# Kernel tuning notes

Hardware: AMD Instinct MI355X
Metric: run time of the kernel (lower is better)

The kernel has to match this reference:

```python
import jax, jax.numpy as jnp
import numpy as np

B, H, W = 2, 192, 192
DIM, HEADS, WS = 192, 6, 16
NT, RD, GS = 128, 20, 128
MLP_HID, TD_F, KS = 384, 48, 5
EPS = 1e-5


def _layernorm(x, g, b):
    m = jnp.mean(x, -1, keepdims=True)
    v = jnp.var(x, -1, keepdims=True)
    return (x - m) / jnp.sqrt(v + EPS) * g + b


def _l2n(x):
    return x / jnp.maximum(jnp.linalg.norm(x, axis=-1, keepdims=True), 1e-12)


def _rpi(ws):
    coords = np.stack(np.meshgrid(np.arange(ws), np.arange(ws), indexing='ij'))
    cf = coords.reshape(2, -1)
    rc = (cf[:, :, None] - cf[:, None, :]).transpose(1, 2, 0)
    rc[..., 0] += ws - 1
    rc[..., 1] += ws - 1
    rc[..., 0] *= 2 * ws - 1
    return rc.sum(-1)  # (ws*ws, ws*ws)


RPI = _rpi(WS)


def _win_attn(qkv, rpb, proj_w, h, w):
    # plain W-MSA (shift_size = 0 -> no mask, no roll)
    b, n, c3 = qkv.shape
    c = c3 // 3
    hd = c // HEADS
    nw = WS * WS
    xw = qkv.reshape(b, h // WS, WS, w // WS, WS, c3).transpose(0, 1, 3, 2, 4, 5).reshape(-1, nw, c3)
    bw = xw.shape[0]
    q, k, v = xw.reshape(bw, nw, 3, HEADS, hd).transpose(2, 0, 3, 1, 4)
    attn = (q * hd ** -0.5) @ k.swapaxes(-2, -1)  # (bw, heads, nw, nw)
    bias = rpb[RPI.reshape(-1)].reshape(nw, nw, HEADS).transpose(2, 0, 1)
    attn = jax.nn.softmax(attn + bias[None])
    out = (attn @ v).swapaxes(1, 2).reshape(bw, nw, c) @ proj_w
    out = out.reshape(b, h // WS, w // WS, WS, WS, c).transpose(0, 1, 3, 2, 4, 5).reshape(b, n, c)
    return out


def _atd_ca(x, td, wq, wk, wv, scale_p):
    q = _l2n(x @ wq)   # (b,n,rd)
    k = _l2n(td @ wk)  # (b,m,rd)
    v = td @ wv        # (b,m,c)
    scale = 1.0 + jnp.clip(scale_p, 0.0, 3.0) * np.log(NT)
    attn = jax.nn.softmax((q @ k.swapaxes(-2, -1)) * scale)  # (b,n,m)
    return attn @ v, attn


def _ac_msa(qkv, tk_id, proj_w):
    b, n, c3 = qkv.shape
    c = c3 // 3
    gs = min(n, GS)
    ng = (n + gs - 1) // gs
    pad = ng * gs - n
    idx = jnp.argsort(tk_id, axis=-1)          # sort tokens by category id
    inv = jnp.argsort(idx, axis=-1)            # inverse permutation
    sq = jnp.take_along_axis(qkv, idx[..., None], axis=1)
    if pad > 0:
        sq = jnp.concatenate([sq, sq[:, n - pad:n][:, ::-1]], axis=1)
    q, k, v = sq.reshape(b, ng, gs, 3, HEADS, c // HEADS).transpose(3, 0, 1, 4, 2, 5)
    attn = jax.nn.softmax((q @ k.swapaxes(-2, -1)) * (c // HEADS) ** -0.5)
    out = (attn @ v).transpose(0, 1, 3, 2, 4).reshape(b, ng * gs, c)[:, :n]
    out = jnp.take_along_axis(out, inv[..., None], axis=1)
    return out @ proj_w


def _convffn(x, x_td, w1, dw, w2, h, w):
    y = jnp.concatenate([jax.nn.gelu(x @ w1, approximate=False), x_td], axis=-1)
    b, n, ch = y.shape
    img = y.swapaxes(1, 2).reshape(b, ch, h, w)
    p = (KS - 1) // 2
    conv = jax.lax.conv_general_dilated(img, dw, (1, 1), [(p, p), (p, p)],
                                        dimension_numbers=('NCHW', 'OIHW', 'NCHW'),
                                        feature_group_count=ch)
    conv = jax.nn.gelu(conv, approximate=False).reshape(b, ch, n).swapaxes(1, 2)
    return (y + conv) @ w2


def setup_inputs():
    key = jax.random.key(0)
    ks = jax.random.split(key, 16)
    p = lambda k, s: jax.random.normal(k, s, jnp.float32) * 0.02
    return {
        'x': jax.random.normal(ks[0], (B, H * W, DIM), jnp.float32),
        'td': jax.random.normal(ks[1], (B, NT, DIM), jnp.float32),
        'norm1_g': jnp.ones((DIM,), jnp.float32), 'norm1_b': jnp.zeros((DIM,), jnp.float32),
        'norm2_g': jnp.ones((DIM,), jnp.float32), 'norm2_b': jnp.zeros((DIM,), jnp.float32),
        'wqkv': p(ks[2], (DIM, 3 * DIM)),
        'rpb': p(ks[3], ((2 * WS - 1) ** 2, HEADS)),
        'win_proj': p(ks[4], (DIM, DIM)),
        'atd_wq': p(ks[5], (DIM, RD)),
        'atd_wk': p(ks[6], (DIM, RD)),
        'atd_wv': p(ks[7], (DIM, DIM)),
        'atd_scale': jnp.ones((1,), jnp.float32),
        'aca_proj': p(ks[8], (DIM, DIM)),
        'fc_td_w': p(ks[9], (DIM, TD_F)),
        'ffn_w1': p(ks[10], (DIM, MLP_HID)),
        'ffn_dw': p(ks[11], (MLP_HID + TD_F, 1, KS, KS)),
        'ffn_w2': p(ks[12], (MLP_HID + TD_F, DIM)),
        'h': H, 'w': W,
    }


def reference(x, td, norm1_g, norm1_b, norm2_g, norm2_b, wqkv, rpb, win_proj,
              atd_wq, atd_wk, atd_wv, atd_scale, aca_proj, fc_td_w,
              ffn_w1, ffn_dw, ffn_w2, h, w):
    shortcut = x
    xn = _layernorm(x, norm1_g, norm1_b)
    qkv = xn @ wqkv  # (b, n, 3c)
    x_atd, sim = _atd_ca(xn, td, atd_wq, atd_wk, atd_wv, atd_scale)
    x_aca = _ac_msa(qkv, jnp.argmax(sim, axis=-1), aca_proj)
    x_win = _win_attn(qkv, rpb, win_proj, h, w)
    x = shortcut + x_win + x_atd + x_aca
    x_td = sim @ (td @ fc_td_w)  # (b, n, td_f): dictionary features routed by cross-attn weights
    x = x + _convffn(_layernorm(x, norm2_g, norm2_b), x_td, ffn_w1, ffn_dw, ffn_w2, h, w)
    return x
```

## Files before the change

kernel.cpp:

```cpp
#include <hip/hip_runtime.h>
#include <hip/hip_bf16.h>
#include <math.h>

#define NTOK 36864
#define NTOT 73728
#define CDIM 192
#define C3   576
#define NH   6
#define HD   32
#define RD   20
#define NTD  128
#define GSZ  128
#define NGRP 288
#define MLP  384
#define TDF  48
#define CH   432
#define RAWLD 384

typedef __hip_bfloat16 bf16;
typedef __attribute__((ext_vector_type(8))) short short8;
typedef __attribute__((ext_vector_type(4))) float f32x4;

__device__ __forceinline__ float gelu_f(float x) {
    float u = x * (1.5957691216f + 0.0713548162f * x * x);
    return x / (1.0f + __expf(-u));
}

__device__ __forceinline__ unsigned short f32_to_bf16u(float f) {
    unsigned int u = __float_as_uint(f);
    u = (u + 0x7FFFu + ((u >> 16) & 1u)) >> 16;
    return (unsigned short)u;
}

__device__ __forceinline__ unsigned pack2bf(float a, float b) {
    return (unsigned)f32_to_bf16u(a) | ((unsigned)f32_to_bf16u(b) << 16);
}

__device__ __forceinline__ float bfbits2f(unsigned short u) {
    return __uint_as_float(((unsigned)u) << 16);
}

__global__ void pack_bt(const float* __restrict__ src, bf16* __restrict__ dst,
                        int K, int N, int ldk, int koff) {
    int i = blockIdx.x * 256 + threadIdx.x;
    if (i >= K * N) return;
    int k = i / N, n = i - k * N;
    dst[(long)n * ldk + koff + k] = __float2bfloat16(src[i]);
}

template<int WF32>
__global__ void ln_kernel(const float* __restrict__ x, const float* __restrict__ g,
                          const float* __restrict__ be, float* __restrict__ outf,
                          bf16* __restrict__ outh) {
    long tok = (long)blockIdx.x * 4 + (threadIdx.x >> 6);
    int lane = threadIdx.x & 63;
    const float* row = x + tok * CDIM;
    float v0 = row[lane], v1 = row[lane + 64], v2 = row[lane + 128];
    float s  = v0 + v1 + v2;
    float ss = v0 * v0 + v1 * v1 + v2 * v2;
    #pragma unroll
    for (int o = 32; o > 0; o >>= 1) {
        s  += __shfl_down(s, o);
        ss += __shfl_down(ss, o);
    }
    s = __shfl(s, 0); ss = __shfl(ss, 0);
    float mean = s * (1.0f / 192.0f);
    float var  = ss * (1.0f / 192.0f) - mean * mean;
    float rstd = rsqrtf(var + 1e-5f);
    float r0 = (v0 - mean) * rstd * g[lane]       + be[lane];
    float r1 = (v1 - mean) * rstd * g[lane + 64]  + be[lane + 64];
    float r2 = (v2 - mean) * rstd * g[lane + 128] + be[lane + 128];
    if (WF32) {
        float* orow = outf + tok * CDIM;
        orow[lane] = r0; orow[lane + 64] = r1; orow[lane + 128] = r2;
    }
    bf16* hrow = outh + tok * CDIM;
    hrow[lane]       = __float2bfloat16(r0);
    hrow[lane + 64]  = __float2bfloat16(r1);
    hrow[lane + 128] = __float2bfloat16(r2);
}

#define LDT 72
template<int ACC, int GELU, int BF16OUT, int CHUNK8, int ADDX, int PL8OUT = 0>
__global__ void __launch_bounds__(256) gemm_bt(
        const bf16* __restrict__ A, const bf16* __restrict__ Bt,
        void* __restrict__ Cv, const float* __restrict__ Xadd,
        int M, int N, int K, int lda, int ldbt, int ldc) {
    __shared__ short As[128 * LDT];
    __shared__ short Bs[64 * LDT];
    int tid  = threadIdx.x;
    int lane = tid & 63;
    int w    = tid >> 6;
    int wr = w >> 1, wc = w & 1;
    int row0 = blockIdx.y * 128, col0 = blockIdx.x * 64;
    int fr = lane & 15, fq = lane >> 4;
    f32x4 acc[4][2];
    #pragma unroll
    for (int m = 0; m < 4; ++m)
        #pragma unroll
        for (int n = 0; n < 2; ++n) acc[m][n] = (f32x4)(0.0f);

    int sa_row = tid >> 3;
    int sa_kc  = (tid & 7) * 8;
    int sb_col = tid & 63;
    int sb_kb  = (tid >> 6) * 16;
    bool cok = (col0 + sb_col) < N;

    for (int k0 = 0; k0 < K; k0 += 64) {
        __syncthreads();
        int kk = k0 + sa_kc;
        #pragma unroll
        for (int p = 0; p < 4; ++p) {
            int r = sa_row + p * 32;
            short8 v = (short8)(0);
            if (kk + 8 <= K) {
                const bf16* src;
                if (CHUNK8)
                    src = A + ((long)(kk >> 3) * NTOT + row0 + r) * 8;
                else
                    src = A + (long)(row0 + r) * lda + kk;
                v = *(const short8*)src;
            } else if (!CHUNK8 && kk < K) {
                #pragma unroll
                for (int i = 0; i < 8; ++i)
                    v[i] = (kk + i < K) ? *(const short*)&A[(long)(row0 + r) * lda + kk + i]
                                        : (short)0;
            }
            *(short8*)&As[r * LDT + sa_kc] = v;
        }
        {
            short8 v0 = (short8)(0), v1 = (short8)(0);
            if (cok) {
                const bf16* src = Bt + (long)(col0 + sb_col) * ldbt + k0 + sb_kb;
                v0 = *(const short8*)src;
                v1 = *(const short8*)(src + 8);
            }
            *(short8*)&Bs[sb_col * LDT + sb_kb]     = v0;
            *(short8*)&Bs[sb_col * LDT + sb_kb + 8] = v1;
        }
        __syncthreads();
        short8 af[4][2], bf_[2][2];
        #pragma unroll
        for (int m = 0; m < 4; ++m) {
            int r = wr * 64 + m * 16 + fr;
            af[m][0] = *(const short8*)&As[r * LDT + fq * 8];
            af[m][1] = *(const short8*)&As[r * LDT + 32 + fq * 8];
        }
        #pragma unroll
        for (int n = 0; n < 2; ++n) {
            int c = wc * 32 + n * 16 + fr;
            bf_[n][0] = *(const short8*)&Bs[c * LDT + fq * 8];
            bf_[n][1] = *(const short8*)&Bs[c * LDT + 32 + fq * 8];
        }
        #pragma unroll
        for (int m = 0; m < 4; ++m)
            #pragma unroll
            for (int n = 0; n < 2; ++n) {
                acc[m][n] = __builtin_amdgcn_mfma_f32_16x16x32_bf16(
                                af[m][0], bf_[n][0], acc[m][n], 0, 0, 0);
                acc[m][n] = __builtin_amdgcn_mfma_f32_16x16x32_bf16(
                                af[m][1], bf_[n][1], acc[m][n], 0, 0, 0);
            }
    }
    #pragma unroll
    for (int m = 0; m < 4; ++m) {
        #pragma unroll
        for (int n = 0; n < 2; ++n) {
            int gc = col0 + wc * 32 + n * 16 + fr;
            if (gc >= N) continue;
            #pragma unroll
            for (int r = 0; r < 4; ++r) {
                int gr = row0 + wr * 64 + m * 16 + fq * 4 + r;
                float vv = acc[m][n][r];
                if (GELU) vv = gelu_f(vv);
                if (BF16OUT) {
                    long o;
                    if (PL8OUT) o = ((long)(gc >> 3) * NTOT + gr) * 8 + (gc & 7);
                    else        o = (long)gr * ldc + gc;
                    ((bf16*)Cv)[o] = __float2bfloat16(vv);
                } else {
                    long o = (long)gr * ldc + gc;
                    float* Cc = (float*)Cv;
                    if (ADDX) Cc[o] = Xadd[o] + vv;
                    else if (ACC) Cc[o] += vv;
                    else Cc[o] = vv;
                }
            }
        }
    }
}

template<int ACC, int GELU>
__global__ void __launch_bounds__(256) gemm_kernel(
        const float* __restrict__ A, const float* __restrict__ B,
        float* __restrict__ Cc, int M, int N, int K, int lda, int ldb, int ldc) {
    __shared__ float As[16][68];
    __shared__ float Bs[16][68];
    int tid = threadIdx.x;
    int tr = tid >> 4, tc = tid & 15;
    int row0 = blockIdx.y * 64, col0 = blockIdx.x * 64;
    float acc[4][4] = {};
    int lm = tid >> 4;
    int lk = tid & 15;
    int bk = tid >> 6;
    int bn = tid & 63;
    for (int k0 = 0; k0 < K; k0 += 16) {
        #pragma unroll
        for (int i = 0; i < 4; ++i) {
            int m = lm + i * 16;
            int gr = row0 + m;
            As[lk][m] = (gr < M) ? A[(long)gr * lda + (k0 + lk)] : 0.0f;
        }
        #pragma unroll
        for (int i = 0; i < 4; ++i) {
            int kk = bk + i * 4;
            int gc = col0 + bn;
            Bs[kk][bn] = (gc < N) ? B[(long)(k0 + kk) * ldb + gc] : 0.0f;
        }
        __syncthreads();
        #pragma unroll
        for (int kk = 0; kk < 16; ++kk) {
            float4 av = *(const float4*)&As[kk][tr * 4];
            float4 bv = *(const float4*)&Bs[kk][tc * 4];
            float a[4] = {av.x, av.y, av.z, av.w};
            float b[4] = {bv.x, bv.y, bv.z, bv.w};
            #pragma unroll
            for (int i = 0; i < 4; ++i)
                #pragma unroll
                for (int j = 0; j < 4; ++j)
                    acc[i][j] = fmaf(a[i], b[j], acc[i][j]);
        }
        __syncthreads();
    }
    #pragma unroll
    for (int i = 0; i < 4; ++i) {
        int gr = row0 + tr * 4 + i;
        if (gr >= M) continue;
        #pragma unroll
        for (int j = 0; j < 4; ++j) {
            int gc = col0 + tc * 4 + j;
            if (gc >= N) continue;
            float v = acc[i][j];
            if (GELU) v = gelu_f(v);
            long o = (long)gr * ldc + gc;
            if (ACC) Cc[o] += v; else Cc[o] = v;
        }
    }
}

__global__ void __launch_bounds__(256) qn_kernel(
        const float* __restrict__ xn, const float* __restrict__ awq,
        float* __restrict__ qn) {
    __shared__ float aw[192 * RD];
    __shared__ float xs[256 * 33];
    int tid = threadIdx.x;
    long tok0 = (long)blockIdx.x * 256;
    for (int e = tid; e < 192 * RD; e += 256) aw[e] = awq[e];
    float acc[RD];
    #pragma unroll
    for (int j = 0; j < RD; ++j) acc[j] = 0.0f;
    for (int kc = 0; kc < 192; kc += 32) {
        __syncthreads();
        for (int e = tid; e < 256 * 32; e += 256) {
            int tk = e >> 5, kk = e & 31;
            xs[tk * 33 + kk] = xn[(tok0 + tk) * CDIM + kc + kk];
        }
        __syncthreads();
        #pragma unroll 8
        for (int kk = 0; kk < 32; ++kk) {
            float v = xs[tid * 33 + kk];
            const float* ar = &aw[(kc + kk) * RD];
            #pragma unroll
            for (int j = 0; j < RD; ++j) acc[j] = fmaf(v, ar[j], acc[j]);
        }
    }
    float ss = 0.0f;
    #pragma unroll
    for (int j = 0; j < RD; ++j) ss += acc[j] * acc[j];
    float inv = 1.0f / fmaxf(sqrtf(ss), 1e-12f);
    float* orow = qn + (tok0 + tid) * RD;
    #pragma unroll
    for (int j = 0; j < RD; ++j) orow[j] = acc[j] * inv;
}

__global__ void l2n_kernel(float* __restrict__ d, int nrows) {
    int i = blockIdx.x * blockDim.x + threadIdx.x;
    if (i >= nrows) return;
    float* r = d + (long)i * RD;
    float ss = 0.0f;
    #pragma unroll
    for (int k = 0; k < RD; ++k) ss += r[k] * r[k];
    float inv = 1.0f / fmaxf(sqrtf(ss), 1e-12f);
    #pragma unroll
    for (int k = 0; k < RD; ++k) r[k] *= inv;
}

__global__ void __launch_bounds__(128) sim_kernel(
        const float* __restrict__ qn, const float* __restrict__ kn,
        const float* __restrict__ scale_p, bf16* __restrict__ sim,
        int* __restrict__ tkid) {
    int tok = blockIdx.x;
    int b = tok / NTOK;
    int j = threadIdx.x;
    __shared__ float qv[RD];
    __shared__ float wred[4];
    __shared__ int   wredi[2];
    if (j < RD) qv[j] = qn[(long)tok * RD + j];
    __syncthreads();
    const float* kr = kn + ((long)b * NTD + j) * RD;
    float s = 0.0f;
    #pragma unroll
    for (int r = 0; r < RD; ++r) s = fmaf(qv[r], kr[r], s);
    float scl = 1.0f + fminf(fmaxf(scale_p[0], 0.0f), 3.0f) * logf(128.0f);
    s *= scl;
    float m = s; int mi = j;
    #pragma unroll
    for (int o = 32; o > 0; o >>= 1) {
        float om = __shfl_down(m, o); int oi = __shfl_down(mi, o);
        if (om > m || (om == m && oi < mi)) { m = om; mi = oi; }
    }
    int wv = j >> 6;
    if ((j & 63) == 0) { wred[wv] = m; wredi[wv] = mi; }
    __syncthreads();
    float m0 = wred[0], m1 = wred[1];
    float gm; int gi;
    if (m1 > m0) { gm = m1; gi = wredi[1]; } else { gm = m0; gi = wredi[0]; }
    float p = __expf(s - gm);
    float t = p;
    #pragma unroll
    for (int o = 32; o > 0; o >>= 1) t += __shfl_down(t, o);
    if ((j & 63) == 0) wred[2 + wv] = t;
    __syncthreads();
    float tot = wred[2] + wred[3];
    sim[(long)tok * NTD + j] = __float2bfloat16(p / tot);
    if (j == 0) tkid[tok] = gi;
}

__global__ void hist_kernel(const int* __restrict__ tkid, int* __restrict__ hist) {
    int tile = blockIdx.x;
    int tid = threadIdx.x;
    __shared__ int h[NTD];
    h[tid] = 0;
    __syncthreads();
    atomicAdd(&h[tkid[tile * GSZ + tid]], 1);
    __syncthreads();
    hist[tile * NTD + tid] = h[tid];
}

__global__ void scan_kernel(int* __restrict__ hist) {
    int b = blockIdx.x;
    int c = threadIdx.x;
    __shared__ int tot[NTD];
    __shared__ int base[NTD];
    int run = 0;
    for (int t = 0; t < NGRP; ++t) {
        int id = (b * NGRP + t) * NTD + c;
        int v = hist[id];
        hist[id] = run;
        run += v;
    }
    tot[c] = run;
    __syncthreads();
    if (c == 0) {
        int a = 0;
        for (int i = 0; i < NTD; ++i) { base[i] = a; a += tot[i]; }
    }
    __syncthreads();
    int bc = base[c];
    for (int t = 0; t < NGRP; ++t)
        hist[(b * NGRP + t) * NTD + c] += bc;
}

__global__ void scatter_kernel(const int* __restrict__ tkid, const int* __restrict__ hist,
                               int* __restrict__ idxs) {
    int tile = blockIdx.x;
    int b = tile / NGRP;
    int gl = tile % NGRP;
    int tid = threadIdx.x;
    __shared__ int cats[GSZ];
    int cat = tkid[tile * GSZ + tid];
    cats[tid] = cat;
    __syncthreads();
    int rank = 0;
    for (int j = 0; j < tid; ++j) rank += (cats[j] == cat) ? 1 : 0;
    int pos = hist[tile * NTD + cat] + rank;
    idxs[b * NTOK + pos] = gl * GSZ + tid;
}

#define VLDW 264
#define VLDA 136


__global__ void __launch_bounds__(256) win_mfma(
        const bf16* __restrict__ qkv, const float* __restrict__ rpb,
        bf16* __restrict__ raw) {
    int t2  = blockIdx.x;
    int h   = t2 % NH;
    int wid = t2 / NH;
    int b = wid / 144;
    int wrem = wid % 144;
    int wy = wrem / 12, wx = wrem % 12;
    long base_tok = (long)b * NTOK;

    __shared__ short Kt[256 * 40];
    __shared__ short Vt[32 * VLDW];
    __shared__ float rb[961];

    int tid = threadIdx.x;
    int lane = tid & 63;
    int wv = tid >> 6;
    int fr = lane & 15, fq = lane >> 4;
    const float scl = 0.17677669529663687f;

    for (int i = tid; i < 961; i += 256) rb[i] = rpb[i * NH + h];

    short8 qf[4];
    #pragma unroll
    for (int m = 0; m < 4; ++m) {
        int q = wv * 64 + m * 16 + fr;
        long nq = base_tok + (long)(wy * 16 + (q >> 4)) * 192 + (wx * 16 + (q & 15));
        qf[m] = *(const short8*)(qkv + nq * C3 + h * HD + fq * 8);
    }

    {
        int s_ = tid >> 2, ch = tid & 3;
        #pragma unroll
        for (int t = 0; t < 4; ++t) {
            int p = t * 64 + s_;
            long nk = base_tok + (long)(wy * 16 + (p >> 4)) * 192 + (wx * 16 + (p & 15));
            const bf16* kb = qkv + nk * C3 + CDIM + h * HD + ch * 8;
            *(short8*)&Kt[p * 40 + ch * 8] = *(const short8*)kb;
            short8 vv = *(const short8*)(kb + CDIM);
            #pragma unroll
            for (int i = 0; i < 8; ++i)
                Vt[(ch * 8 + i) * VLDW + p] = vv[i];
        }
    }
    __syncthreads();

    f32x4 acc[4][2];
    float lst[4];
    #pragma unroll
    for (int m = 0; m < 4; ++m) {
        acc[m][0] = (f32x4)(0.0f); acc[m][1] = (f32x4)(0.0f);
        lst[m] = 0.0f;
    }

    for (int t = 0; t < 4; ++t) {
        short8 ak[4], av[2][2];
        #pragma unroll
        for (int c = 0; c < 4; ++c)
            ak[c] = *(const short8*)&Kt[(t * 64 + c * 16 + fr) * 40 + fq * 8];
        #pragma unroll
        for (int n = 0; n < 2; ++n)
            #pragma unroll
            for (int ks = 0; ks < 2; ++ks)
                av[n][ks] = *(const short8*)&Vt[(n * 16 + fr) * VLDW + t * 64 + ks * 32 + fq * 8];

        #pragma unroll
        for (int m = 0; m < 4; ++m) {
            int q = wv * 64 + m * 16 + fr;
            int iy = q >> 4, ix = q & 15;
            int bxb = ix + 15 - 4 * fq;
            float s[4][4];
            #pragma unroll
            for (int c = 0; c < 4; ++c) {
                f32x4 s4 = (f32x4)(0.0f);
                s4 = __builtin_amdgcn_mfma_f32_16x16x32_bf16(ak[c], qf[m], s4, 0, 0, 0);
                const float* rbp = &rb[(iy + 15 - (t * 4 + c)) * 31 + bxb];
                #pragma unroll
                for (int r = 0; r < 4; ++r)
                    s[c][r] = s4[r] * scl + rbp[-r];
            }
            float ps = 0.0f;
            #pragma unroll
            for (int c = 0; c < 4; ++c)
                #pragma unroll
                for (int r = 0; r < 4; ++r) {
                    float p = __expf(s[c][r]);
                    s[c][r] = p;
                    ps += p;
                }
            ps += __shfl_xor(ps, 16);
            ps += __shfl_xor(ps, 32);
            lst[m] += ps;
            unsigned pk[4][2];
            #pragma unroll
            for (int c = 0; c < 4; ++c) {
                pk[c][0] = pack2bf(s[c][0], s[c][1]);
                pk[c][1] = pack2bf(s[c][2], s[c][3]);
            }
            #pragma unroll
            for (int ks = 0; ks < 2; ++ks) {
                unsigned u[4];
                #pragma unroll
                for (int jj = 0; jj < 4; ++jj) {
                    int src = fr + 16 * (2 * (fq & 1) + (jj >> 1));
                    unsigned lo = (unsigned)__shfl((int)pk[2 * ks][jj & 1], src);
                    unsigned hi = (unsigned)__shfl((int)pk[2 * ks + 1][jj & 1], src);
                    u[jj] = (fq & 2) ? hi : lo;
                }
                short8 pb;
                #pragma unroll
                for (int jj = 0; jj < 4; ++jj) {
                    pb[2 * jj]     = (short)(u[jj] & 0xFFFF);
                    pb[2 * jj + 1] = (short)(u[jj] >> 16);
                }
                #pragma unroll
                for (int n = 0; n < 2; ++n)
                    acc[m][n] = __builtin_amdgcn_mfma_f32_16x16x32_bf16(
                                    av[n][ks], pb, acc[m][n], 0, 0, 0);
            }
        }
    }
    #pragma unroll
    for (int m = 0; m < 4; ++m) {
        int q = wv * 64 + m * 16 + fr;
        long nq = base_tok + (long)(wy * 16 + (q >> 4)) * 192 + (wx * 16 + (q & 15));
        float inv = 1.0f / lst[m];
        #pragma unroll
        for (int n = 0; n < 2; ++n) {
            uint2 wv2;
            wv2.x = pack2bf(acc[m][n][0] * inv, acc[m][n][1] * inv);
            wv2.y = pack2bf(acc[m][n][2] * inv, acc[m][n][3] * inv);
            *(uint2*)(raw + nq * RAWLD + h * HD + n * 16 + 4 * fq) = wv2;
        }
    }
}

__global__ void __launch_bounds__(128) aca_mfma(
        const bf16* __restrict__ qkv, const int* __restrict__ idxs,
        bf16* __restrict__ raw) {
    int t2   = blockIdx.x;
    int h    = t2 % NH;
    int grp  = t2 / NH;
    int b = grp / NGRP;
    int g = grp % NGRP;
    long btok = (long)b * NTOK;

    __shared__ short Kt[128 * 40];
    __shared__ short Vt[32 * VLDA];
    __shared__ int   sidx[GSZ];

    int tid = threadIdx.x;
    int lane = tid & 63;
    int half = tid >> 6;
    int fr = lane & 15, fq = lane >> 4;
    const float scl = 0.17677669529663687f;

    sidx[tid] = idxs[btok + g * GSZ + tid];
    __syncthreads();

    short8 qf[4];
    #pragma unroll
    for (int m = 0; m < 4; ++m) {
        long n = btok + sidx[half * 64 + m * 16 + fr];
        qf[m] = *(const short8*)(qkv + n * C3 + h * HD + fq * 8);
    }

    {
        int s_ = tid >> 1, hf = tid & 1;
        int d0 = hf * 16;
        #pragma unroll
        for (int t = 0; t < 2; ++t) {
            int p = t * 64 + s_;
            long n = btok + sidx[p];
            const bf16* kb = qkv + n * C3 + CDIM + h * HD + d0;
            *(short8*)&Kt[p * 40 + d0]     = *(const short8*)kb;
            *(short8*)&Kt[p * 40 + d0 + 8] = *(const short8*)(kb + 8);
            short8 v0 = *(const short8*)(kb + CDIM);
            short8 v1 = *(const short8*)(kb + CDIM + 8);
            #pragma unroll
            for (int i = 0; i < 8; ++i) {
                Vt[(d0 + i) * VLDA + p]     = v0[i];
                Vt[(d0 + 8 + i) * VLDA + p] = v1[i];
            }
        }
    }
    __syncthreads();

    f32x4 acc[4][2];
    float lst[4];
    #pragma unroll
    for (int m = 0; m < 4; ++m) {
        acc[m][0] = (f32x4)(0.0f); acc[m][1] = (f32x4)(0.0f);
        lst[m] = 0.0f;
    }

    for (int t = 0; t < 2; ++t) {
        short8 ak[4], av[2][2];
        #pragma unroll
        for (int c = 0; c < 4; ++c)
            ak[c] = *(const short8*)&Kt[(t * 64 + c * 16 + fr) * 40 + fq * 8];
        #pragma unroll
        for (int n = 0; n < 2; ++n)
            #pragma unroll
            for (int ks = 0; ks < 2; ++ks)
                av[n][ks] = *(const short8*)&Vt[(n * 16 + fr) * VLDA + t * 64 + ks * 32 + fq * 8];

        #pragma unroll
        for (int m = 0; m < 4; ++m) {
            float s[4][4];
            #pragma unroll
            for (int c = 0; c < 4; ++c) {
                f32x4 s4 = (f32x4)(0.0f);
                s4 = __builtin_amdgcn_mfma_f32_16x16x32_bf16(ak[c], qf[m], s4, 0, 0, 0);
                #pragma unroll
                for (int r = 0; r < 4; ++r) s[c][r] = s4[r] * scl;
            }
            float ps = 0.0f;
            #pragma unroll
            for (int c = 0; c < 4; ++c)
                #pragma unroll
                for (int r = 0; r < 4; ++r) {
                    float p = __expf(s[c][r]);
                    s[c][r] = p;
                    ps += p;
                }
            ps += __shfl_xor(ps, 16);
            ps += __shfl_xor(ps, 32);
            lst[m] += ps;
            unsigned pk[4][2];
            #pragma unroll
            for (int c = 0; c < 4; ++c) {
                pk[c][0] = pack2bf(s[c][0], s[c][1]);
                pk[c][1] = pack2bf(s[c][2], s[c][3]);
            }
            #pragma unroll
            for (int ks = 0; ks < 2; ++ks) {
                unsigned u[4];
                #pragma unroll
                for (int jj = 0; jj < 4; ++jj) {
                    int src = fr + 16 * (2 * (fq & 1) + (jj >> 1));
                    unsigned lo = (unsigned)__shfl((int)pk[2 * ks][jj & 1], src);
                    unsigned hi = (unsigned)__shfl((int)pk[2 * ks + 1][jj & 1], src);
                    u[jj] = (fq & 2) ? hi : lo;
                }
                short8 pb;
                #pragma unroll
                for (int jj = 0; jj < 4; ++jj) {
                    pb[2 * jj]     = (short)(u[jj] & 0xFFFF);
                    pb[2 * jj + 1] = (short)(u[jj] >> 16);
                }
                #pragma unroll
                for (int n = 0; n < 2; ++n)
                    acc[m][n] = __builtin_amdgcn_mfma_f32_16x16x32_bf16(
                                    av[n][ks], pb, acc[m][n], 0, 0, 0);
            }
        }
    }
    #pragma unroll
    for (int m = 0; m < 4; ++m) {
        long n = btok + sidx[half * 64 + m * 16 + fr];
        float inv = 1.0f / lst[m];
        #pragma unroll
        for (int nn = 0; nn < 2; ++nn) {
            uint2 wv2;
            wv2.x = pack2bf(acc[m][nn][0] * inv, acc[m][nn][1] * inv);
            wv2.y = pack2bf(acc[m][nn][2] * inv, acc[m][nn][3] * inv);
            *(uint2*)(raw + n * RAWLD + CDIM + h * HD + nn * 16 + 4 * fq) = wv2;
        }
    }
}

__global__ void xtdcopy_kernel(const bf16* __restrict__ xtd, bf16* __restrict__ y) {
    long tok = (long)blockIdx.x * 256 + threadIdx.x;
    const uint4* src = (const uint4*)(xtd + tok * TDF);
    #pragma unroll
    for (int j = 0; j < 6; ++j)
        *(uint4*)(y + ((long)(48 + j) * NTOT + tok) * 8) = src[j];
}

#define CPS 1296
__global__ void __launch_bounds__(256) conv_kernel(
        const bf16* __restrict__ y, const float* __restrict__ dw,
        bf16* __restrict__ zc) {
    int bid = blockIdx.x;
    int ck   = bid % 54;
    int tile = (bid / 54) % 36;
    int b    = bid / (54 * 36);
    int ty = tile / 6, tx = tile % 6;
    int c0 = ck * 8;
    __shared__ float ys[8 * CPS];
    __shared__ float wt[8 * 25];
    int tid = threadIdx.x;
    const bf16* ypl = y + ((long)ck * NTOT + (long)b * NTOK) * 8;
    for (int p = tid; p < 1296; p += 256) {
        int ly = p / 36, lx = p - ly * 36;
        int gy = ty * 32 + ly - 2, gx = tx * 32 + lx - 2;
        float f[8];
        if (gy >= 0 && gy < 192 && gx >= 0 && gx < 192) {
            short8 hv = *(const short8*)(ypl + (long)(gy * 192 + gx) * 8);
            #pragma unroll
            for (int i = 0; i < 8; ++i) f[i] = bfbits2f((unsigned short)hv[i]);
        } else {
            #pragma unroll
            for (int i = 0; i < 8; ++i) f[i] = 0.0f;
        }
        #pragma unroll
        for (int i = 0; i < 8; ++i) ys[i * CPS + p] = f[i];
    }
    for (int e = tid; e < 200; e += 256) wt[e] = dw[c0 * 25 + e];
    __syncthreads();
    int col = tid & 31, r4 = tid >> 5;
    int py0 = r4 * 4;
    long tok0 = (long)b * NTOK + (long)(ty * 32 + py0) * 192 + tx * 32 + col;
    unsigned hh[4][4];
    for (int c = 0; c < 8; ++c) {
        const float* yc = &ys[c * CPS];
        float w[25];
        #pragma unroll
        for (int t = 0; t < 25; ++t) w[t] = wt[c * 25 + t];
        float a[4] = {0.0f, 0.0f, 0.0f, 0.0f};
        #pragma unroll
        for (int dy2 = 0; dy2 < 8; ++dy2) {
            float rv[5];
            #pragma unroll
            for (int dx = 0; dx < 5; ++dx)
                rv[dx] = yc[(py0 + dy2) * 36 + col + dx];
            #pragma unroll
            for (int i = 0; i < 4; ++i) {
                int dy = dy2 - i;
                if (dy >= 0 && dy < 5) {
                    #pragma unroll
                    for (int dx = 0; dx < 5; ++dx)
                        a[i] = fmaf(rv[dx], w[dy * 5 + dx], a[i]);
                }
            }
        }
        #pragma unroll
        for (int i = 0; i < 4; ++i) {
            float center = yc[(py0 + i + 2) * 36 + col + 2];
            unsigned short hsh = f32_to_bf16u(center + gelu_f(a[i]));
            if (c & 1) hh[i][c >> 1] |= ((unsigned)hsh) << 16;
            else       hh[i][c >> 1] = (unsigned)hsh;
        }
    }
    #pragma unroll
    for (int i = 0; i < 4; ++i) {
        long tok = tok0 + (long)i * 192;
        *(uint4*)(zc + ((long)ck * NTOT + tok) * 8) =
            make_uint4(hh[i][0], hh[i][1], hh[i][2], hh[i][3]);
    }
}

extern "C" void kernel_launch(void* const* d_in, const int* in_sizes, int n_in,
                              void* d_out, int out_size, void* d_ws, size_t ws_size,
                              hipStream_t stream) {
    (void)in_sizes; (void)n_in; (void)out_size; (void)ws_size;
    const float* x     = (const float*)d_in[0];
    const float* td    = (const float*)d_in[1];
    const float* n1g   = (const float*)d_in[2];
    const float* n1b   = (const float*)d_in[3];
    const float* n2g   = (const float*)d_in[4];
    const float* n2b   = (const float*)d_in[5];
    const float* wqkv  = (const float*)d_in[6];
    const float* rpb   = (const float*)d_in[7];
    const float* wproj = (const float*)d_in[8];
    const float* awq   = (const float*)d_in[9];
    const float* awk   = (const float*)d_in[10];
    const float* awv   = (const float*)d_in[11];
    const float* ascl  = (const float*)d_in[12];
    const float* aproj = (const float*)d_in[13];
    const float* fcw   = (const float*)d_in[14];
    const float* w1    = (const float*)d_in[15];
    const float* dw    = (const float*)d_in[16];
    const float* w2    = (const float*)d_in[17];
    float* out = (float*)d_out;

    char* ws = (char*)d_ws;
    size_t off = 0;
    auto alloc = [&](size_t bytes) -> char* {
        char* p = ws + off;
        off += (bytes + 255) & ~(size_t)255;
        return p;
    };
    bf16*  qkv  = (bf16*)alloc((size_t)NTOT * C3 * 2);
    float* xn   = (float*)alloc((size_t)NTOT * CDIM * 4);
    bf16*  xnh  = (bf16*)alloc((size_t)NTOT * CDIM * 2);
    float* qn   = (float*)alloc((size_t)NTOT * RD * 4);
    bf16*  simb = (bf16*)alloc((size_t)NTOT * NTD * 2);
    bf16*  xtd  = (bf16*)alloc((size_t)NTOT * TDF * 2);
    float* kn   = (float*)alloc((size_t)2 * NTD * RD * 4);
    float* vtd  = (float*)alloc((size_t)2 * NTD * CDIM * 4);
    float* tdf  = (float*)alloc((size_t)2 * NTD * TDF * 4);
    bf16*  vtdT = (bf16*)alloc((size_t)2 * CDIM * NTD * 2);
    bf16*  tdfT = (bf16*)alloc((size_t)2 * TDF * NTD * 2);
    bf16*  wqkvT= (bf16*)alloc((size_t)C3 * CDIM * 2);
    bf16*  projT= (bf16*)alloc((size_t)CDIM * 384 * 2);
    bf16*  w1T  = (bf16*)alloc((size_t)MLP * CDIM * 2);
    bf16*  w2T  = (bf16*)alloc((size_t)CDIM * 448 * 2);
    int*   tkid = (int*)alloc((size_t)NTOT * 4);
    int*   idxs = (int*)alloc((size_t)NTOT * 4);
    int*   hist = (int*)alloc((size_t)576 * NTD * 4);
    bf16*  y    = qkv;
    bf16*  raw  = (bf16*)xn;
    bf16*  zc   = (bf16*)xn;

    pack_bt<<<(192 * 576 + 255) / 256, 256, 0, stream>>>(wqkv, wqkvT, 192, 576, 192, 0);
    pack_bt<<<(192 * 192 + 255) / 256, 256, 0, stream>>>(wproj, projT, 192, 192, 384, 0);
    pack_bt<<<(192 * 192 + 255) / 256, 256, 0, stream>>>(aproj, projT, 192, 192, 384, 192);
    pack_bt<<<(192 * 384 + 255) / 256, 256, 0, stream>>>(w1, w1T, 192, 384, 192, 0);
    hipMemsetAsync(w2T, 0, (size_t)CDIM * 448 * 2, stream);
    pack_bt<<<(432 * 192 + 255) / 256, 256, 0, stream>>>(w2, w2T, 432, 192, 448, 0);

    ln_kernel<1><<<NTOT / 4, 256, 0, stream>>>(x, n1g, n1b, xn, xnh);

    gemm_bt<0,0,1,0,0><<<dim3(9, 576), 256, 0, stream>>>(
        xnh, wqkvT, qkv, nullptr, NTOT, C3, CDIM, CDIM, CDIM, C3);

    qn_kernel<<<NTOT / 256, 256, 0, stream>>>(xn, awq, qn);

    gemm_kernel<0,0><<<dim3(1, 4), 256, 0, stream>>>(td, awk, kn, 2 * NTD, RD, CDIM, CDIM, RD, RD);
    gemm_kernel<0,0><<<dim3(3, 4), 256, 0, stream>>>(td, awv, vtd, 2 * NTD, CDIM, CDIM, CDIM, CDIM, CDIM);
    gemm_kernel<0,0><<<dim3(1, 4), 256, 0, stream>>>(td, fcw, tdf, 2 * NTD, TDF, CDIM, CDIM, TDF, TDF);
    l2n_kernel<<<1, 256, 0, stream>>>(kn, 2 * NTD);
    for (int b = 0; b < 2; ++b) {
        pack_bt<<<(NTD * CDIM + 255) / 256, 256, 0, stream>>>(
            vtd + (size_t)b * NTD * CDIM, vtdT + (size_t)b * CDIM * NTD, NTD, CDIM, NTD, 0);
        pack_bt<<<(NTD * TDF + 255) / 256, 256, 0, stream>>>(
            tdf + (size_t)b * NTD * TDF, tdfT + (size_t)b * TDF * NTD, NTD, TDF, NTD, 0);
    }

    sim_kernel<<<NTOT, 128, 0, stream>>>(qn, kn, ascl, simb, tkid);

    for (int b = 0; b < 2; ++b) {
        gemm_bt<0,0,0,0,1><<<dim3(3, 288), 256, 0, stream>>>(
            simb + (size_t)b * NTOK * NTD, vtdT + (size_t)b * CDIM * NTD,
            out + (size_t)b * NTOK * CDIM, x + (size_t)b * NTOK * CDIM,
            NTOK, CDIM, NTD, NTD, NTD, CDIM);
        gemm_bt<0,0,1,0,0><<<dim3(1, 288), 256, 0, stream>>>(
            simb + (size_t)b * NTOK * NTD, tdfT + (size_t)b * TDF * NTD,
            xtd + (size_t)b * NTOK * TDF, nullptr, NTOK, TDF, NTD, NTD, NTD, TDF);
    }

    hist_kernel<<<576, 128, 0, stream>>>(tkid, hist);
    scan_kernel<<<2, 128, 0, stream>>>(hist);
    scatter_kernel<<<576, 128, 0, stream>>>(tkid, hist, idxs);

    win_mfma<<<288 * NH, 256, 0, stream>>>(qkv, rpb, raw);
    aca_mfma<<<576 * NH, 128, 0, stream>>>(qkv, idxs, raw);
    gemm_bt<1,0,0,0,0><<<dim3(3, 576), 256, 0, stream>>>(
        raw, projT, out, nullptr, NTOT, CDIM, 384, RAWLD, 384, CDIM);

    ln_kernel<0><<<NTOT / 4, 256, 0, stream>>>(out, n2g, n2b, nullptr, xnh);

    gemm_bt<0,1,1,0,0,1><<<dim3(6, 576), 256, 0, stream>>>(
        xnh, w1T, y, nullptr, NTOT, MLP, CDIM, CDIM, CDIM, 0);
    xtdcopy_kernel<<<NTOT / 256, 256, 0, stream>>>(xtd, y);

    conv_kernel<<<2 * 36 * 54, 256, 0, stream>>>(y, dw, zc);
    gemm_bt<1,0,0,1,0><<<dim3(3, 576), 256, 0, stream>>>(
        zc, w2T, out, nullptr, NTOT, CDIM, CH, 0, 448, CDIM);
}
```

Baseline: 771.0 us.

## Parallelize category scan, use wave-per-token sim kernel, fuse weight packing

```diff
diff --git a/kernel.cpp b/kernel.cpp
--- a/kernel.cpp
+++ b/kernel.cpp
@@ -39,6 +39,28 @@
 __device__ __forceinline__ float bfbits2f(unsigned short u) {
     return __uint_as_float(((unsigned)u) << 16);
 }
+
+__global__ void packw_kernel(const float* __restrict__ wqkv, const float* __restrict__ wproj,
+                             const float* __restrict__ aproj, const float* __restrict__ w1,
+                             const float* __restrict__ w2,
+                             bf16* __restrict__ wqkvT, bf16* __restrict__ projT,
+                             bf16* __restrict__ w1T, bf16* __restrict__ w2T) {
+    int i = blockIdx.x * 256 + threadIdx.x;
+    const int S0 = 192 * 576, S1 = 192 * 192, S2 = 192 * 192, S3 = 192 * 384,
+              S4 = 432 * 192, S5 = 192 * 16;
+    if (i < S0) { int k = i / 576, n = i % 576; wqkvT[(long)n * 192 + k] = __float2bfloat16(wqkv[i]); return; }
+    i -= S0;
+    if (i < S1) { int k = i / 192, n = i % 192; projT[(long)n * 384 + k] = __float2bfloat16(wproj[i]); return; }
+    i -= S1;
+    if (i < S2) { int k = i / 192, n = i % 192; projT[(long)n * 384 + 192 + k] = __float2bfloat16(aproj[i]); return; }
+    i -= S2;
+    if (i < S3) { int k = i / 384, n = i % 384; w1T[(long)n * 192 + k] = __float2bfloat16(w1[i]); return; }
+    i -= S3;
+    if (i < S4) { int k = i / 192, n = i % 192; w2T[(long)n * 448 + k] = __float2bfloat16(w2[i]); return; }
+    i -= S4;
+    if (i < S5) { int n = i / 16, k = i % 16; w2T[(long)n * 448 + 432 + k] = __float2bfloat16(0.0f); }
+}
+#define PACKW_TOT (192*576 + 192*192*2 + 192*384 + 432*192 + 192*16)
 
 __global__ void pack_bt(const float* __restrict__ src, bf16* __restrict__ dst,
                         int K, int N, int ldk, int koff) {
@@ -295,45 +317,44 @@
     for (int k = 0; k < RD; ++k) r[k] *= inv;
 }
 
-__global__ void __launch_bounds__(128) sim_kernel(
+__global__ void __launch_bounds__(256) sim_kernel(
         const float* __restrict__ qn, const float* __restrict__ kn,
         const float* __restrict__ scale_p, bf16* __restrict__ sim,
         int* __restrict__ tkid) {
-    int tok = blockIdx.x;
-    int b = tok / NTOK;
-    int j = threadIdx.x;
-    __shared__ float qv[RD];
-    __shared__ float wred[4];
-    __shared__ int   wredi[2];
-    if (j < RD) qv[j] = qn[(long)tok * RD + j];
-    __syncthreads();
-    const float* kr = kn + ((long)b * NTD + j) * RD;
-    float s = 0.0f;
-    #pragma unroll
-    for (int r = 0; r < RD; ++r) s = fmaf(qv[r], kr[r], s);
+    int lane = threadIdx.x & 63;
+    long tok = (long)blockIdx.x * 4 + (threadIdx.x >> 6);
+    int b = (tok >= NTOK) ? 1 : 0;
+    float q[RD];
+    const float* qrow = qn + tok * RD;
+    #pragma unroll
+    for (int r = 0; r < RD; ++r) q[r] = qrow[r];
+    const float* k0 = kn + ((long)b * NTD + lane) * RD;
+    const float* k1 = k0 + 64 * RD;
+    float s0 = 0.0f, s1 = 0.0f;
+    #pragma unroll
+    for (int r = 0; r < RD; ++r) {
+        s0 = fmaf(q[r], k0[r], s0);
+        s1 = fmaf(q[r], k1[r], s1);
+    }
     float scl = 1.0f + fminf(fmaxf(scale_p[0], 0.0f), 3.0f) * logf(128.0f);
-    s *= scl;
-    float m = s; int mi = j;
-    #pragma unroll
-    for (int o = 32; o > 0; o >>= 1) {
-        float om = __shfl_down(m, o); int oi = __shfl_down(mi, o);
+    s0 *= scl; s1 *= scl;
+    float m; int mi;
+    if (s0 >= s1) { m = s0; mi = lane; } else { m = s1; mi = lane + 64; }
+    #pragma unroll
+    for (int o = 1; o < 64; o <<= 1) {
+        float om = __shfl_xor(m, o);
+        int   oi = __shfl_xor(mi, o);
         if (om > m || (om == m && oi < mi)) { m = om; mi = oi; }
     }
-    int wv = j >> 6;
-    if ((j & 63) == 0) { wred[wv] = m; wredi[wv] = mi; }
-    __syncthreads();
-    float m0 = wred[0], m1 = wred[1];
-    float gm; int gi;
-    if (m1 > m0) { gm = m1; gi = wredi[1]; } else { gm = m0; gi = wredi[0]; }
-    float p = __expf(s - gm);
-    float t = p;
-    #pragma unroll
-    for (int o = 32; o > 0; o >>= 1) t += __shfl_down(t, o);
-    if ((j & 63) == 0) wred[2 + wv] = t;
-    __syncthreads();
-    float tot = wred[2] + wred[3];
-    sim[(long)tok * NTD + j] = __float2bfloat16(p / tot);
-    if (j == 0) tkid[tok] = gi;
+    float p0 = __expf(s0 - m), p1 = __expf(s1 - m);
+    float t = p0 + p1;
+    #pragma unroll
+    for (int o = 1; o < 64; o <<= 1) t += __shfl_xor(t, o);
+    float inv = 1.0f / t;
+    bf16* srow = sim + tok * NTD;
+    srow[lane]      = __float2bfloat16(p0 * inv);
+    srow[lane + 64] = __float2bfloat16(p1 * inv);
+    if (lane == 0) tkid[tok] = mi;
 }
 
 __global__ void hist_kernel(const int* __restrict__ tkid, int* __restrict__ hist) {
@@ -347,28 +368,55 @@
     hist[tile * NTD + tid] = h[tid];
 }
 
-__global__ void scan_kernel(int* __restrict__ hist) {
-    int b = blockIdx.x;
-    int c = threadIdx.x;
-    __shared__ int tot[NTD];
-    __shared__ int base[NTD];
-    int run = 0;
-    for (int t = 0; t < NGRP; ++t) {
-        int id = (b * NGRP + t) * NTD + c;
-        int v = hist[id];
-        hist[id] = run;
-        run += v;
-    }
-    tot[c] = run;
+__global__ void __launch_bounds__(64) scan1_kernel(int* __restrict__ hist,
+                                                   int* __restrict__ tot) {
+    int bc = blockIdx.x;
+    int b = bc >> 7, c = bc & (NTD - 1);
+    int lane = threadIdx.x;
+    if (lane < 32) {
+        int base = (b * NGRP + lane * 9) * NTD + c;
+        int v[9];
+        int s = 0;
+        #pragma unroll
+        for (int k = 0; k < 9; ++k) { v[k] = hist[base + k * NTD]; s += v[k]; }
+        int run = s;
+        #pragma unroll
+        for (int o = 1; o < 32; o <<= 1) {
+            int t = __shfl_up(run, o);
+            if (lane >= o) run += t;
+        }
+        if (lane == 31) tot[bc] = run;
+        int acc = run - s;
+        #pragma unroll
+        for (int k = 0; k < 9; ++k) { hist[base + k * NTD] = acc; acc += v[k]; }
+    }
+}
+
+__global__ void __launch_bounds__(128) scan2_kernel(const int* __restrict__ tot,
+                                                    int* __restrict__ basev) {
+    int b = blockIdx.x, c = threadIdx.x;
+    int lane = c & 63, wv = c >> 6;
+    int s = tot[b * NTD + c];
+    int run = s;
+    #pragma unroll
+    for (int o = 1; o < 64; o <<= 1) {
+        int t = __shfl_up(run, o);
+        if (lane >= o) run += t;
+    }
+    __shared__ int wsum[2];
+    if (lane == 63) wsum[wv] = run;
     __syncthreads();
-    if (c == 0) {
-        int a = 0;
-        for (int i = 0; i < NTD; ++i) { base[i] = a; a += tot[i]; }
-    }
-    __syncthreads();
-    int bc = base[c];
-    for (int t = 0; t < NGRP; ++t)
-        hist[(b * NGRP + t) * NTD + c] += bc;
+    int add = (wv == 1) ? wsum[0] : 0;
+    basev[b * NTD + c] = run - s + add;
+}
+
+__global__ void __launch_bounds__(256) scan3_kernel(int* __restrict__ hist,
+                                                    const int* __restrict__ basev) {
+    int i = blockIdx.x * 256 + threadIdx.x;
+    int c = i & (NTD - 1);
+    int bt = i >> 7;
+    int b = (bt >= NGRP) ? 1 : 0;
+    hist[i] += basev[b * NTD + c];
 }
 
 __global__ void scatter_kernel(const int* __restrict__ tkid, const int* __restrict__ hist,
@@ -793,16 +841,14 @@
     int*   tkid = (int*)alloc((size_t)NTOT * 4);
     int*   idxs = (int*)alloc((size_t)NTOT * 4);
     int*   hist = (int*)alloc((size_t)576 * NTD * 4);
+    int*   tot  = (int*)alloc((size_t)2 * NTD * 4);
+    int*   basev= (int*)alloc((size_t)2 * NTD * 4);
     bf16*  y    = qkv;
     bf16*  raw  = (bf16*)xn;
     bf16*  zc   = (bf16*)xn;
 
-    pack_bt<<<(192 * 576 + 255) / 256, 256, 0, stream>>>(wqkv, wqkvT, 192, 576, 192, 0);
-    pack_bt<<<(192 * 192 + 255) / 256, 256, 0, stream>>>(wproj, projT, 192, 192, 384, 0);
-    pack_bt<<<(192 * 192 + 255) / 256, 256, 0, stream>>>(aproj, projT, 192, 192, 384, 192);
-    pack_bt<<<(192 * 384 + 255) / 256, 256, 0, stream>>>(w1, w1T, 192, 384, 192, 0);
-    hipMemsetAsync(w2T, 0, (size_t)CDIM * 448 * 2, stream);
-    pack_bt<<<(432 * 192 + 255) / 256, 256, 0, stream>>>(w2, w2T, 432, 192, 448, 0);
+    packw_kernel<<<(PACKW_TOT + 255) / 256, 256, 0, stream>>>(
+        wqkv, wproj, aproj, w1, w2, wqkvT, projT, w1T, w2T);
 
     ln_kernel<1><<<NTOT / 4, 256, 0, stream>>>(x, n1g, n1b, xn, xnh);
 
@@ -822,7 +868,7 @@
             tdf + (size_t)b * NTD * TDF, tdfT + (size_t)b * TDF * NTD, NTD, TDF, NTD, 0);
     }
 
-    sim_kernel<<<NTOT, 128, 0, stream>>>(qn, kn, ascl, simb, tkid);
+    sim_kernel<<<NTOT / 4, 256, 0, stream>>>(qn, kn, ascl, simb, tkid);
 
     for (int b = 0; b < 2; ++b) {
         gemm_bt<0,0,0,0,1><<<dim3(3, 288), 256, 0, stream>>>(
@@ -835,7 +881,9 @@
     }
 
     hist_kernel<<<576, 128, 0, stream>>>(tkid, hist);
-    scan_kernel<<<2, 128, 0, stream>>>(hist);
+    scan1_kernel<<<2 * NTD, 64, 0, stream>>>(hist, tot);
+    scan2_kernel<<<2, 128, 0, stream>>>(tot, basev);
+    scan3_kernel<<<(2 * NGRP * NTD) / 256, 256, 0, stream>>>(hist, basev);
     scatter_kernel<<<576, 128, 0, stream>>>(tkid, hist, idxs);
 
     win_mfma<<<288 * NH, 256, 0, stream>>>(qkv, rpb, raw);
```

Result: faster. 738.3 us (-4.2%).
